# Kernel tuning notes

Hardware: AMD Instinct MI355X
Metric: run time of the kernel (lower is better)

The kernel has to match this reference:

```python
import jax, jax.numpy as jnp
import numpy as np

NEG = -9e15  # mask value from original (-9000000000000000.0)

def setup_inputs() -> dict:
    key = jax.random.key(0)
    k1, k2, k3, k4 = jax.random.split(key, 4)
    N, nin, nout = 8192, 256, 128
    h = jax.random.normal(k1, (N, nin), dtype=jnp.float32)
    adj = jax.random.randint(k2, (N, N), 0, 2, dtype=jnp.int32)
    w = jax.random.normal(k3, (nin, nout), dtype=jnp.float32)
    v = jax.random.normal(k4, (2 * nout, 1), dtype=jnp.float32)
    return {"h": h, "adj": adj, "w": w, "v": v}

def reference(h, adj, w, v):
    nout = w.shape[1]
    hw = h @ w                      # [N, nout]
    hw1 = hw @ v[:nout]             # [N, 1]
    hw2 = hw @ v[nout:]             # [N, 1]
    eij = hw1 + hw2.T               # [N, N] additive outer-sum scores
    att = jnp.where(adj > 0, eij, jnp.float32(NEG))
    att = jax.nn.softmax(att, axis=1)
    return att @ hw                 # [N, nout]
```

## Files before the change

kernel.cpp:

```cpp
#include <hip/hip_runtime.h>
#include <math.h>

#define N_ROWS 8192
#define NIN    256
#define NOUT   128
#define CUTOFF 45.0f

__global__ __launch_bounds__(256) void k_wv(const float* __restrict__ w,
                                            const float* __restrict__ v,
                                            float* __restrict__ wv) {
    int k = threadIdx.x;
    const float* wr = w + (size_t)k * NOUT;
    const float* v2 = v + NOUT;
    float acc = 0.f;
#pragma unroll
    for (int n = 0; n < NOUT; n += 4) {
        float4 a = *(const float4*)(wr + n);
        float4 b = *(const float4*)(v2 + n);
        acc = fmaf(a.x, b.x, acc);
        acc = fmaf(a.y, b.y, acc);
        acc = fmaf(a.z, b.z, acc);
        acc = fmaf(a.w, b.w, acc);
    }
    wv[k] = acc;
}

__global__ __launch_bounds__(256) void k_s(const float* __restrict__ h,
                                           const float* __restrict__ wv,
                                           float* __restrict__ s) {
    int wid  = threadIdx.x >> 6;
    int lane = threadIdx.x & 63;
    int i = blockIdx.x * 4 + wid;
    const float* hr = h + (size_t)i * NIN;
    float acc = 0.f;
#pragma unroll
    for (int u = 0; u < NIN; u += 64)
        acc = fmaf(hr[lane + u], wv[lane + u], acc);
#pragma unroll
    for (int off = 32; off > 0; off >>= 1)
        acc += __shfl_down(acc, off, 64);
    if (lane == 0) s[i] = acc;
}

__global__ __launch_bounds__(256) void k_gemm(const float* __restrict__ h,
                                              const float* __restrict__ w,
                                              float* __restrict__ hw) {
    __shared__ float hT[64][36];
    __shared__ float wT[64][128];

    int tid  = threadIdx.x;
    int row0 = blockIdx.x * 32;
    int tr = tid >> 5;
    int tc = tid & 31;

    float acc[4][4] = {};

    for (int k0 = 0; k0 < NIN; k0 += 64) {
#pragma unroll
        for (int q = 0; q < 2; ++q) {
            int f  = tid + q * 256;
            int r  = f >> 4;
            int kq = f & 15;
            float4 hv = *(const float4*)(h + (size_t)(row0 + r) * NIN + k0 + kq * 4);
            hT[kq * 4 + 0][r] = hv.x;
            hT[kq * 4 + 1][r] = hv.y;
            hT[kq * 4 + 2][r] = hv.z;
            hT[kq * 4 + 3][r] = hv.w;
        }
#pragma unroll
        for (int q = 0; q < 8; ++q) {
            int f  = tid + q * 256;
            int kk = f >> 5;
            int cq = f & 31;
            *(float4*)(&wT[kk][cq * 4]) =
                *(const float4*)(w + (size_t)(k0 + kk) * NOUT + cq * 4);
        }
        __syncthreads();

#pragma unroll 8
        for (int kk = 0; kk < 64; ++kk) {
            float4 av = *(const float4*)(&hT[kk][tr * 4]);
            float4 bv = *(const float4*)(&wT[kk][tc * 4]);
            float a4[4] = {av.x, av.y, av.z, av.w};
            float b4[4] = {bv.x, bv.y, bv.z, bv.w};
#pragma unroll
            for (int rr = 0; rr < 4; ++rr)
#pragma unroll
                for (int cc = 0; cc < 4; ++cc)
                    acc[rr][cc] = fmaf(a4[rr], b4[cc], acc[rr][cc]);
        }
        __syncthreads();
    }

#pragma unroll
    for (int rr = 0; rr < 4; ++rr) {
        float4 o = make_float4(acc[rr][0], acc[rr][1], acc[rr][2], acc[rr][3]);
        *(float4*)(hw + (size_t)(row0 + tr * 4 + rr) * NOUT + tc * 4) = o;
    }
}

__global__ __launch_bounds__(256) void k_att(const int* __restrict__ adj,
                                             const float* __restrict__ s_g,
                                             const float* __restrict__ hw,
                                             float* __restrict__ out) {
    __shared__ unsigned short idxs[N_ROWS];
    __shared__ float wmax[4];
    __shared__ int cnt;

    int i   = blockIdx.x;
    int tid = threadIdx.x;
    const int* arow = adj + (size_t)i * N_ROWS;

    if (tid == 0) cnt = 0;

    float sv[32];
    unsigned int mask = 0;
    float m = -INFINITY;
#pragma unroll
    for (int u = 0; u < 8; ++u) {
        int j0 = u * 1024 + tid * 4;
        int4   a  = *(const int4*)(arow + j0);
        float4 sx = *(const float4*)(s_g + j0);
        sv[u * 4 + 0] = sx.x;
        sv[u * 4 + 1] = sx.y;
        sv[u * 4 + 2] = sx.z;
        sv[u * 4 + 3] = sx.w;
        if (a.x > 0) { mask |= 1u << (u * 4 + 0); m = fmaxf(m, sx.x); }
        if (a.y > 0) { mask |= 1u << (u * 4 + 1); m = fmaxf(m, sx.y); }
        if (a.z > 0) { mask |= 1u << (u * 4 + 2); m = fmaxf(m, sx.z); }
        if (a.w > 0) { mask |= 1u << (u * 4 + 3); m = fmaxf(m, sx.w); }
    }

#pragma unroll
    for (int off = 32; off > 0; off >>= 1)
        m = fmaxf(m, __shfl_down(m, off, 64));
    if ((tid & 63) == 0) wmax[tid >> 6] = m;
    __syncthreads();
    m = fmaxf(fmaxf(wmax[0], wmax[1]), fmaxf(wmax[2], wmax[3]));

    float thresh = m - CUTOFF;
#pragma unroll
    for (int u = 0; u < 32; ++u) {
        if ((mask >> u) & 1u) {
            float sj = sv[u];
            if (sj >= thresh) {
                int pos = atomicAdd(&cnt, 1);
                idxs[pos] = (unsigned short)((u >> 2) * 1024 + tid * 4 + (u & 3));
            }
        }
    }
    __syncthreads();
    int n = cnt;

    if (tid < NOUT) {
        float acc = 0.f, den = 0.f;
        if (n > 0) {
            for (int e = 0; e < n; ++e) {
                int j   = idxs[e];
                float p = __expf(s_g[j] - m);
                acc = fmaf(p, hw[(size_t)j * NOUT + tid], acc);
                den += p;
            }
        } else {
            for (int j = 0; j < N_ROWS; ++j)
                acc += hw[(size_t)j * NOUT + tid];
            den = (float)N_ROWS;
        }
        out[(size_t)i * NOUT + tid] = acc / den;
    }
}

extern "C" void kernel_launch(void* const* d_in, const int* in_sizes, int n_in,
                              void* d_out, int out_size, void* d_ws, size_t ws_size,
                              hipStream_t stream) {
    const float* h   = (const float*)d_in[0];
    const int*   adj = (const int*)  d_in[1];
    const float* w   = (const float*)d_in[2];
    const float* v   = (const float*)d_in[3];
    float* out = (float*)d_out;

    char* ws = (char*)d_ws;
    float* hw = (float*)(ws);
    float* s  = (float*)(ws + (size_t)N_ROWS * NOUT * 4);
    float* wv = (float*)(ws + (size_t)N_ROWS * NOUT * 4 + (size_t)N_ROWS * 4);

    k_wv  <<<1,    256, 0, stream>>>(w, v, wv);
    k_s   <<<N_ROWS / 4, 256, 0, stream>>>(h, wv, s);
    k_gemm<<<N_ROWS / 32, 256, 0, stream>>>(h, w, hw);
    k_att <<<N_ROWS, 256, 0, stream>>>(adj, s, hw, out);
}
```

Measured before the change: 384.8 us.

## Precompute global top-score candidate list to skip scanning full adjacency rows

Softmax weights depend only on the column score s_j, so a new single-block kernel binary-searches a threshold at the 32nd-largest score and records every column within the cutoff of it. The attention kernel then reads adjacency entries only for those candidate columns to find the row max and the surviving indices. It falls back to the old full-row scan when the row max is too low for the candidate list to be complete. This removes most of the full reads of the int32 adjacency matrix, at the cost of one serial single-block kernel and scattered gathers into the adjacency rows.

After: 378.9 us. No clear change (-1.5%).

```diff
diff --git a/kernel.cpp b/kernel.cpp
--- a/kernel.cpp
+++ b/kernel.cpp
@@ -5,6 +5,18 @@
 #define NIN    256
 #define NOUT   128
 #define CUTOFF 45.0f
+#define TOPK   32
+
+__device__ __forceinline__ float block_max_256(float v, float* red) {
+#pragma unroll
+    for (int off = 32; off > 0; off >>= 1)
+        v = fmaxf(v, __shfl_down(v, off, 64));
+    if ((threadIdx.x & 63) == 0) red[threadIdx.x >> 6] = v;
+    __syncthreads();
+    float r = fmaxf(fmaxf(red[0], red[1]), fmaxf(red[2], red[3]));
+    __syncthreads();
+    return r;
+}
 
 __global__ __launch_bounds__(256) void k_wv(const float* __restrict__ w,
                                             const float* __restrict__ v,
@@ -40,6 +52,46 @@
     for (int off = 32; off > 0; off >>= 1)
         acc += __shfl_down(acc, off, 64);
     if (lane == 0) s[i] = acc;
+}
+
+__global__ __launch_bounds__(256) void k_top(const float* __restrict__ s_g,
+                                             int* __restrict__ L,
+                                             int* __restrict__ nL_p,
+                                             float* __restrict__ T_p) {
+    __shared__ float sd[N_ROWS];
+    __shared__ float red[4];
+    __shared__ int c;
+    int tid = threadIdx.x;
+    float mloc = -INFINITY;
+    for (int j = tid; j < N_ROWS; j += 256) {
+        float v = s_g[j];
+        sd[j] = v;
+        mloc = fmaxf(mloc, v);
+    }
+    __syncthreads();
+    float mstar = block_max_256(mloc, red);
+    float lo = mstar - 300.0f, hi = mstar;
+    for (int it = 0; it < 22; ++it) {
+        float t = 0.5f * (lo + hi);
+        if (tid == 0) c = 0;
+        __syncthreads();
+        int cl = 0;
+        for (int j = tid; j < N_ROWS; j += 256) cl += (sd[j] >= t) ? 1 : 0;
+#pragma unroll
+        for (int off = 32; off > 0; off >>= 1) cl += __shfl_down(cl, off, 64);
+        if ((tid & 63) == 0) atomicAdd(&c, cl);
+        __syncthreads();
+        if (c >= TOPK) lo = t; else hi = t;
+        __syncthreads();
+    }
+    float T = lo - CUTOFF;
+    if (tid == 0) { *T_p = T; c = 0; }
+    __syncthreads();
+    for (int j = tid; j < N_ROWS; j += 256) {
+        if (sd[j] >= T) { int p = atomicAdd(&c, 1); L[p] = j; }
+    }
+    __syncthreads();
+    if (tid == 0) *nL_p = c;
 }
 
 __global__ __launch_bounds__(256) void k_gemm(const float* __restrict__ h,
@@ -99,54 +151,61 @@
     }
 }
 
-__global__ __launch_bounds__(256) void k_att(const int* __restrict__ adj,
-                                             const float* __restrict__ s_g,
-                                             const float* __restrict__ hw,
-                                             float* __restrict__ out) {
+__global__ __launch_bounds__(256) void k_att2(const int* __restrict__ adj,
+                                              const float* __restrict__ s_g,
+                                              const float* __restrict__ hw,
+                                              const int* __restrict__ L,
+                                              const int* __restrict__ nL_p,
+                                              const float* __restrict__ T_p,
+                                              float* __restrict__ out) {
     __shared__ unsigned short idxs[N_ROWS];
-    __shared__ float wmax[4];
+    __shared__ float red[4];
     __shared__ int cnt;
 
     int i   = blockIdx.x;
     int tid = threadIdx.x;
+    if (tid == 0) cnt = 0;
+    int   nL = nL_p[0];
+    float T  = T_p[0];
     const int* arow = adj + (size_t)i * N_ROWS;
 
-    if (tid == 0) cnt = 0;
-
-    float sv[32];
-    unsigned int mask = 0;
-    float m = -INFINITY;
-#pragma unroll
-    for (int u = 0; u < 8; ++u) {
-        int j0 = u * 1024 + tid * 4;
-        int4   a  = *(const int4*)(arow + j0);
-        float4 sx = *(const float4*)(s_g + j0);
-        sv[u * 4 + 0] = sx.x;
-        sv[u * 4 + 1] = sx.y;
-        sv[u * 4 + 2] = sx.z;
-        sv[u * 4 + 3] = sx.w;
-        if (a.x > 0) { mask |= 1u << (u * 4 + 0); m = fmaxf(m, sx.x); }
-        if (a.y > 0) { mask |= 1u << (u * 4 + 1); m = fmaxf(m, sx.y); }
-        if (a.z > 0) { mask |= 1u << (u * 4 + 2); m = fmaxf(m, sx.z); }
-        if (a.w > 0) { mask |= 1u << (u * 4 + 3); m = fmaxf(m, sx.w); }
-    }
-
-#pragma unroll
-    for (int off = 32; off > 0; off >>= 1)
-        m = fmaxf(m, __shfl_down(m, off, 64));
-    if ((tid & 63) == 0) wmax[tid >> 6] = m;
-    __syncthreads();
-    m = fmaxf(fmaxf(wmax[0], wmax[1]), fmaxf(wmax[2], wmax[3]));
-
-    float thresh = m - CUTOFF;
-#pragma unroll
-    for (int u = 0; u < 32; ++u) {
-        if ((mask >> u) & 1u) {
-            float sj = sv[u];
-            if (sj >= thresh) {
-                int pos = atomicAdd(&cnt, 1);
-                idxs[pos] = (unsigned short)((u >> 2) * 1024 + tid * 4 + (u & 3));
+    float mloc = -INFINITY;
+    for (int t = tid; t < nL; t += 256) {
+        int j = L[t];
+        if (arow[j] > 0) mloc = fmaxf(mloc, s_g[j]);
+    }
+    float m = block_max_256(mloc, red);
+
+    if (m - CUTOFF >= T) {
+        for (int t = tid; t < nL; t += 256) {
+            int j = L[t];
+            if (arow[j] > 0) {
+                float sj = s_g[j];
+                if (sj >= m - CUTOFF) {
+                    int p = atomicAdd(&cnt, 1);
+                    idxs[p] = (unsigned short)j;
+                }
             }
+        }
+    } else {
+        float m2 = -INFINITY;
+        for (int j0 = tid * 4; j0 < N_ROWS; j0 += 1024) {
+            int4   a  = *(const int4*)(arow + j0);
+            float4 sx = *(const float4*)(s_g + j0);
+            if (a.x > 0) m2 = fmaxf(m2, sx.x);
+            if (a.y > 0) m2 = fmaxf(m2, sx.y);
+            if (a.z > 0) m2 = fmaxf(m2, sx.z);
+            if (a.w > 0) m2 = fmaxf(m2, sx.w);
+        }
+        m = block_max_256(m2, red);
+        float th = m - CUTOFF;
+        for (int j0 = tid * 4; j0 < N_ROWS; j0 += 1024) {
+            int4   a  = *(const int4*)(arow + j0);
+            float4 sx = *(const float4*)(s_g + j0);
+            if (a.x > 0 && sx.x >= th) { int p = atomicAdd(&cnt, 1); idxs[p] = (unsigned short)(j0 + 0); }
+            if (a.y > 0 && sx.y >= th) { int p = atomicAdd(&cnt, 1); idxs[p] = (unsigned short)(j0 + 1); }
+            if (a.z > 0 && sx.z >= th) { int p = atomicAdd(&cnt, 1); idxs[p] = (unsigned short)(j0 + 2); }
+            if (a.w > 0 && sx.w >= th) { int p = atomicAdd(&cnt, 1); idxs[p] = (unsigned short)(j0 + 3); }
         }
     }
     __syncthreads();
@@ -181,11 +240,16 @@
 
     char* ws = (char*)d_ws;
     float* hw = (float*)(ws);
-    float* s  = (float*)(ws + (size_t)N_ROWS * NOUT * 4);
-    float* wv = (float*)(ws + (size_t)N_ROWS * NOUT * 4 + (size_t)N_ROWS * 4);
-
-    k_wv  <<<1,    256, 0, stream>>>(w, v, wv);
-    k_s   <<<N_ROWS / 4, 256, 0, stream>>>(h, wv, s);
+    size_t o  = (size_t)N_ROWS * NOUT * 4;
+    float* s  = (float*)(ws + o);   o += (size_t)N_ROWS * 4;
+    float* wv = (float*)(ws + o);   o += (size_t)NIN * 4;
+    int*   L  = (int*)  (ws + o);   o += (size_t)N_ROWS * 4;
+    int*   nL = (int*)  (ws + o);   o += 16;
+    float* T  = (float*)(ws + o);
+
+    k_wv  <<<1,           256, 0, stream>>>(w, v, wv);
+    k_s   <<<N_ROWS / 4,  256, 0, stream>>>(h, wv, s);
+    k_top <<<1,           256, 0, stream>>>(s, L, nL, T);
     k_gemm<<<N_ROWS / 32, 256, 0, stream>>>(h, w, hw);
-    k_att <<<N_ROWS, 256, 0, stream>>>(adj, s, hw, out);
-}
+    k_att2<<<N_ROWS,      256, 0, stream>>>(adj, s, hw, L, nL, T, out);
+}
```
